# Optimization experiments

Hardware: AMD Instinct MI355X
Metric: run time of the kernel (lower is better)

Reference implementation:

```python
import jax, jax.numpy as jnp
import numpy as np

B, NPQ, NPV, NSL, K, ED, H = 64, 1024, 256, 1, 128, 16, 8
DK = K // H  # per-head dim (k_dim = v_dim = emb_dim // num_heads)
ETYPES = [("PQ","PQ"),("PQ","PV"),("PQ","Slack"),("PV","PQ"),("PV","PV"),("PV","Slack"),("Slack","PQ"),("Slack","PV")]
ECOUNTS = [262144, 131072, 4096, 131072, 65536, 2048, 4096, 2048]
NN = {"PQ": B*NPQ, "PV": B*NPV, "Slack": B*NSL}
LN_EPS = 1e-5


def setup_inputs() -> dict:
    ks = iter(jax.random.split(jax.random.key(0), 64))
    inp = {}
    for name, n in [("x_PQ", NN["PQ"]), ("x_PV", NN["PV"]), ("x_Slack", NN["Slack"])]:
        inp[name] = jax.random.normal(next(ks), (n, K), jnp.float32)
    for t, ((s, d), E) in enumerate(zip(ETYPES, ECOUNTS)):
        src = jax.random.randint(next(ks), (E,), 0, NN[s])
        dst = jax.random.randint(next(ks), (E,), 0, NN[d])
        inp[f"ei_{t}"] = jnp.stack([src, dst]).astype(jnp.int32)
        inp[f"ea_{t}"] = jax.random.normal(next(ks), (E, ED), jnp.float32)
    sc = 1.0 / np.sqrt(K)
    shapes = {"Wk": (2,8,K,K), "bk": (2,8,K), "Wq": (2,8,K,K), "bq": (2,8,K),
              "Wv": (2,8,K,K), "bv": (2,8,K), "Ws": (2,8,K,K), "bconv": (2,8,K),
              "We": (2,8,ED,K), "be": (2,8,K), "Wgt": (K,K), "bgt": (K,),
              "Wq1": (K,K), "Wk2": (K,K), "Wv2": (K,K), "Wo": (K,K), "bo": (K,)}
    for name, sh in shapes.items():
        inp[name] = jax.random.normal(next(ks), sh, jnp.float32) * sc
    inp["ln_g"] = jnp.ones((K,), jnp.float32)
    inp["ln_b"] = jnp.zeros((K,), jnp.float32)
    return inp


def _cross_attention(x1, x2, Wq1, Wk2, Wv2, Wo, bo):
    # x1: [B, N1, K] queries; x2: [B, N2, K] keys/values
    Bq, N1, _ = x1.shape
    N2 = x2.shape[1]
    q = (x1 @ Wq1).reshape(Bq, N1, H, DK)
    k = (x2 @ Wk2).reshape(Bq, N2, H, DK)
    v = (x2 @ Wv2).reshape(Bq, N2, H, DK)
    attn = jnp.einsum("bnhd,bmhd->bhnm", q, k) / np.sqrt(DK).astype(np.float32)
    attn = jax.nn.softmax(attn, axis=-1)
    out = jnp.einsum("bhnm,bmhd->bnhd", attn, v).reshape(Bq, N1, H * DK)
    return out @ Wo + bo


def _forward(x_PQ, x_PV, x_Slack, ei, ea,
             Wk, bk, Wq, bq, Wv, bv, Ws, bconv, We, be,
             Wgt, bgt, Wq1, Wk2, Wv2, Wo, bo, ln_g, ln_b):
    x = {"PQ": x_PQ, "PV": x_PV, "Slack": x_Slack}
    # global feature from input node features
    gf = jnp.concatenate([x_PQ.reshape(B, NPQ, K),
                          x_PV.reshape(B, NPV, K),
                          x_Slack.reshape(B, NSL, K)], axis=1)
    gf = gf @ Wgt + bgt
    gnode = jnp.concatenate([gf.mean(axis=1, keepdims=True),
                             gf.max(axis=1, keepdims=True)], axis=1)  # [B, 2, K]
    # 2 HeteroConv layers of ResGatedGraphConv, aggr='sum' over edge types
    for l in range(2):
        new = {t: jnp.zeros((NN[t], K), x_PQ.dtype) for t in ("PQ", "PV", "Slack")}
        for t, (s, d) in enumerate(ETYPES):
            xs, xd = x[s], x[d]
            k_ = xd @ Wk[l, t] + bk[l, t]   # lin_key on dst
            q_ = xs @ Wq[l, t] + bq[l, t]   # lin_query on src
            v_ = xs @ Wv[l, t] + bv[l, t]   # lin_value on src
            e_ = ea[t] @ We[l, t] + be[l, t]  # lin_edge
            si, di = ei[t][0], ei[t][1]
            gate = jax.nn.sigmoid(k_[di] + q_[si] + e_)  # [E, K]
            agg = jax.ops.segment_sum(gate * v_[si], di, num_segments=NN[d])
            new[d] = new[d] + agg + xd @ Ws[l, t] + bconv[l, t]
        x = {t: jax.nn.relu(v) for t, v in new.items()}
    # cross-attention vs. global mean/max nodes, residual, layernorm (PQ, PV only)
    res = {}
    for key2, N1 in (("PQ", NPQ), ("PV", NPV)):
        x1 = x[key2].reshape(B, N1, K)
        ca = _cross_attention(x1, gnode, Wq1, Wk2, Wv2, Wo, bo).reshape(B * N1, K)
        h = x[key2] + ca
        mu = h.mean(axis=-1, keepdims=True)
        var = ((h - mu) ** 2).mean(axis=-1, keepdims=True)
        res[key2] = (h - mu) * jax.lax.rsqrt(var + LN_EPS) * ln_g + ln_b
    return res["PQ"], res["PV"], x["Slack"]


def reference(x_PQ, x_PV, x_Slack,
              ei_0, ei_1, ei_2, ei_3, ei_4, ei_5, ei_6, ei_7,
              ea_0, ea_1, ea_2, ea_3, ea_4, ea_5, ea_6, ea_7,
              Wk, bk, Wq, bq, Wv, bv, Ws, bconv, We, be,
              Wgt, bgt, Wq1, Wk2, Wv2, Wo, bo, ln_g, ln_b):
    ei = [ei_0, ei_1, ei_2, ei_3, ei_4, ei_5, ei_6, ei_7]
    ea = [ea_0, ea_1, ea_2, ea_3, ea_4, ea_5, ea_6, ea_7]
    return _forward(x_PQ, x_PV, x_Slack, ei, ea,
                    Wk, bk, Wq, bq, Wv, bv, Ws, bconv, We, be,
                    Wgt, bgt, Wq1, Wk2, Wv2, Wo, bo, ln_g, ln_b)
```

## Files before the change

kernel.cpp:

```cpp
#include <hip/hip_runtime.h>
#include <hip/hip_bf16.h>
#include <math.h>

#define N_PQ 65536
#define N_PV 16384
#define N_SL 64

typedef __attribute__((ext_vector_type(8))) short s16x8;
typedef __attribute__((ext_vector_type(4))) float f32x4;

__device__ __forceinline__ ushort f2bf(float f) {
    union { float f; unsigned u; } x; x.f = f;
    unsigned r = x.u + 0x7fff + ((x.u >> 16) & 1);
    return (ushort)(r >> 16);
}
__device__ __forceinline__ float bf2f(ushort u) {
    union { unsigned u; float f; } x; x.u = ((unsigned)u) << 16;
    return x.f;
}

template<int OUT_BF16>
__global__ __launch_bounds__(256) void gemm_mfma(
    const ushort* __restrict__ A, const ushort* __restrict__ Bt,
    const float* __restrict__ bias, void* __restrict__ Cv, int M, int N)
{
    __shared__ ushort As[128 * 128];
    const int tid = threadIdx.x;
    const int m0 = blockIdx.x * 128;
    const int n0 = blockIdx.y * 128;

    #pragma unroll
    for (int p = 0; p < 8; ++p) {
        int c = p * 256 + tid;
        int row = c >> 4, c16 = c & 15;
        int gr = m0 + row;
        int4 v = make_int4(0, 0, 0, 0);
        if (gr < M) v = *(const int4*)(A + (size_t)gr * 128 + c16 * 8);
        *(int4*)(As + row * 128 + (c16 ^ (row & 7)) * 8) = v;
    }
    __syncthreads();

    const int lane = tid & 63, wave = tid >> 6;
    const int wr = wave >> 1, wc = wave & 1;
    const int lrow = lane & 15, lk = lane >> 4;

    f32x4 acc[4][4];
    #pragma unroll
    for (int mi = 0; mi < 4; ++mi)
        #pragma unroll
        for (int ni = 0; ni < 4; ++ni) acc[mi][ni] = (f32x4){0.f, 0.f, 0.f, 0.f};

    #pragma unroll
    for (int kk = 0; kk < 4; ++kk) {
        s16x8 a[4], b[4];
        #pragma unroll
        for (int mi = 0; mi < 4; ++mi) {
            int row = wr * 64 + mi * 16 + lrow;
            int c16 = (lk + kk * 4) ^ (row & 7);
            a[mi] = *(const s16x8*)(As + row * 128 + c16 * 8);
        }
        #pragma unroll
        for (int ni = 0; ni < 4; ++ni) {
            int n = n0 + wc * 64 + ni * 16 + lrow;
            b[ni] = *(const s16x8*)(Bt + (size_t)n * 128 + kk * 32 + lk * 8);
        }
        #pragma unroll
        for (int mi = 0; mi < 4; ++mi)
            #pragma unroll
            for (int ni = 0; ni < 4; ++ni)
                acc[mi][ni] = __builtin_amdgcn_mfma_f32_16x16x32_bf16(
                    a[mi], b[ni], acc[mi][ni], 0, 0, 0);
    }

    if (OUT_BF16) {
        __syncthreads();
        ushort* Cl = As;
        #pragma unroll
        for (int mi = 0; mi < 4; ++mi)
            #pragma unroll
            for (int ni = 0; ni < 4; ++ni)
                #pragma unroll
                for (int r = 0; r < 4; ++r) {
                    int row = wr * 64 + mi * 16 + (lane >> 4) * 4 + r;
                    int col = wc * 64 + ni * 16 + (lane & 15);
                    float v = acc[mi][ni][r] + (bias ? bias[n0 + col] : 0.f);
                    Cl[row * 128 + (((col >> 3) ^ (row & 7)) << 3) + (col & 7)] = f2bf(v);
                }
        __syncthreads();
        ushort* C = (ushort*)Cv;
        #pragma unroll
        for (int p = 0; p < 8; ++p) {
            int c = p * 256 + tid;
            int row = c >> 4, c16 = c & 15;
            int gr = m0 + row;
            if (gr < M)
                *(int4*)(C + (size_t)gr * N + n0 + c16 * 8) =
                    *(const int4*)(As + row * 128 + (c16 ^ (row & 7)) * 8);
        }
    } else {
        float* C = (float*)Cv;
        #pragma unroll
        for (int mi = 0; mi < 4; ++mi)
            #pragma unroll
            for (int ni = 0; ni < 4; ++ni)
                #pragma unroll
                for (int r = 0; r < 4; ++r) {
                    int row = m0 + wr * 64 + mi * 16 + (lane >> 4) * 4 + r;
                    int col = n0 + wc * 64 + ni * 16 + (lane & 15);
                    if (row < M)
                        C[(size_t)row * N + col] =
                            acc[mi][ni][r] + (bias ? bias[col] : 0.f);
                }
    }
}

__global__ void prep_mats(
    const float* __restrict__ Wk, const float* __restrict__ Wq,
    const float* __restrict__ Wv, const float* __restrict__ Ws,
    const float* __restrict__ Wgt, const float* __restrict__ Wq1,
    const float* __restrict__ Wk2, const float* __restrict__ Wv2,
    const float* __restrict__ Wo,
    ushort* __restrict__ panels, ushort* __restrict__ wssum,
    ushort* __restrict__ finalw)
{
    const int m = blockIdx.x >> 6;
    const int e = (blockIdx.x & 63) * 256 + threadIdx.x;
    const int nl = e >> 7, k = e & 127;
    const int dstlist[3][3] = {{0,3,6},{1,4,7},{2,5,-1}};
    const int srclist[3][3] = {{0,1,2},{3,4,5},{6,7,-1}};
    const int nkg[3] = {3,3,2};
    const int gofs[3] = {0,1280,2560};

    if (m < 52) {
        int l = m / 26, r = m % 26;
        int g, slot;
        if (r < 10)      { g = 0; slot = r; }
        else if (r < 20) { g = 1; slot = r - 10; }
        else             { g = 2; slot = r - 20; }
        int nk = nkg[g];
        float val; int col;
        if (slot < nk) {
            int t = dstlist[g][slot];
            val = Wk[(size_t)(l * 8 + t) * 16384 + k * 128 + nl];
            col = slot * 128 + nl;
        } else if (slot < 2 * nk) {
            int s = slot - nk; int t = srclist[g][s];
            val = Wq[(size_t)(l * 8 + t) * 16384 + k * 128 + nl];
            col = nk * 128 + s * 256 + ((nl >> 1) << 2) + (nl & 1);
        } else if (slot < 3 * nk) {
            int s = slot - 2 * nk; int t = srclist[g][s];
            val = Wv[(size_t)(l * 8 + t) * 16384 + k * 128 + nl];
            col = nk * 128 + s * 256 + ((nl >> 1) << 2) + 2 + (nl & 1);
        } else {
            float s = 0.f;
            #pragma unroll
            for (int i = 0; i < 3; ++i) {
                int t = dstlist[g][i];
                if (t >= 0) s += Ws[(size_t)(l * 8 + t) * 16384 + k * 128 + nl];
            }
            val = s; col = 1152 + nl;
        }
        panels[((size_t)l * 3328 + gofs[g] + col) * 128 + k] = f2bf(val);
    } else if (m < 54) {
        int l = m - 52;
        float s = Ws[(size_t)(l * 8 + 2) * 16384 + k * 128 + nl]
                + Ws[(size_t)(l * 8 + 5) * 16384 + k * 128 + nl];
        wssum[(size_t)l * 16384 + nl * 128 + k] = f2bf(s);
    } else {
        const float* fsrc[5] = {Wgt, Wq1, Wk2, Wv2, Wo};
        int idx = m - 54;
        finalw[(size_t)idx * 16384 + nl * 128 + k] = f2bf(fsrc[idx][k * 128 + nl]);
    }
}

__global__ void prep_bias(
    const float* __restrict__ bk, const float* __restrict__ bq,
    const float* __restrict__ bv, const float* __restrict__ bconv,
    float* __restrict__ bias_cat, float* __restrict__ bcsum)
{
    const int l = blockIdx.x / 3, g = blockIdx.x % 3;
    const int dstlist[3][3] = {{0,3,6},{1,4,7},{2,5,-1}};
    const int srclist[3][3] = {{0,1,2},{3,4,5},{6,7,-1}};
    const int nkg[3] = {3,3,2};
    const int gofs[3] = {0,1280,2560};
    const int nslots = (g < 2) ? 10 : 6;
    int nk = nkg[g];
    for (int idx = threadIdx.x; idx < nslots * 128; idx += 256) {
        int slot = idx >> 7, nl = idx & 127;
        float val; int col;
        if (slot < nk) {
            int t = dstlist[g][slot];
            val = bk[(l * 8 + t) * 128 + nl];
            col = slot * 128 + nl;
        } else if (slot < 2 * nk) {
            int s = slot - nk; int t = srclist[g][s];
            val = bq[(l * 8 + t) * 128 + nl];
            col = nk * 128 + s * 256 + ((nl >> 1) << 2) + (nl & 1);
        } else if (slot < 3 * nk) {
            int s = slot - 2 * nk; int t = srclist[g][s];
            val = bv[(l * 8 + t) * 128 + nl];
            col = nk * 128 + s * 256 + ((nl >> 1) << 2) + 2 + (nl & 1);
        } else {
            float s = 0.f;
            #pragma unroll
            for (int i = 0; i < 3; ++i) {
                int t = dstlist[g][i];
                if (t >= 0) s += bconv[(l * 8 + t) * 128 + nl];
            }
            val = s; col = 1152 + nl;
        }
        bias_cat[l * 3328 + gofs[g] + col] = val;
    }
    if (g == 2 && threadIdx.x < 128) {
        bcsum[l * 128 + threadIdx.x] =
            bconv[(l * 8 + 2) * 128 + threadIdx.x] + bconv[(l * 8 + 5) * 128 + threadIdx.x];
    }
}

struct HArgs {
    const int* ei[6];
    int E[6];
    int base[6];
    int cum[7];
};

__global__ void hist_kernel(HArgs A, int* __restrict__ bins)
{
    int g = blockIdx.x * 256 + threadIdx.x;
    if (g >= A.cum[6]) return;
    int t = 0;
    #pragma unroll
    for (int i = 0; i < 5; ++i) t += (g >= A.cum[i + 1]);
    int e = g - A.cum[t];
    int dst = A.ei[t][A.E[t] + e];
    atomicAdd(&bins[A.base[t] + dst], 1);
}

__global__ __launch_bounds__(256) void scan_a(
    const int* __restrict__ bins, int* __restrict__ offs, int* __restrict__ bsum)
{
    __shared__ int s[256];
    const int b = blockIdx.x, t = threadIdx.x;
    int v = bins[b * 256 + t];
    s[t] = v; __syncthreads();
    #pragma unroll
    for (int off = 1; off < 256; off <<= 1) {
        int x = (t >= off) ? s[t - off] : 0;
        __syncthreads();
        s[t] += x;
        __syncthreads();
    }
    offs[b * 256 + t] = s[t] - v;
    if (t == 255) bsum[b] = s[255];
}

__global__ __launch_bounds__(1024) void scan_b(
    const int* __restrict__ bsum, int* __restrict__ carry)
{
    __shared__ int s[1024];
    const int t = threadIdx.x;
    int v = bsum[t];
    s[t] = v; __syncthreads();
    for (int off = 1; off < 1024; off <<= 1) {
        int x = (t >= off) ? s[t - off] : 0;
        __syncthreads();
        s[t] += x;
        __syncthreads();
    }
    carry[t] = s[t] - v;
}

__global__ void scan_c(int* __restrict__ offs, const int* __restrict__ carry,
                       int* __restrict__ cursor)
{
    const int b = blockIdx.x, t = threadIdx.x;
    int v = offs[b * 256 + t] + carry[b];
    offs[b * 256 + t] = v;
    cursor[b * 256 + t] = v;
}

__global__ void scatter_kernel(HArgs A, int* __restrict__ cursor,
                               int* __restrict__ lsrc, int* __restrict__ leid)
{
    int g = blockIdx.x * 256 + threadIdx.x;
    if (g >= A.cum[6]) return;
    int t = 0;
    #pragma unroll
    for (int i = 0; i < 5; ++i) t += (g >= A.cum[i + 1]);
    int e = g - A.cum[t];
    int src = A.ei[t][e];
    int dst = A.ei[t][A.E[t] + e];
    int pos = atomicAdd(&cursor[A.base[t] + dst], 1);
    lsrc[pos] = src;
    leid[pos] = e;
}

struct GTA {
    int base, kcol, qvcol, lds;
    const ushort* Ys;
    const float* ea;
    const float* We;
    const float* be;
};
struct GArgs {
    GTA t[3];
    const int* offs;
    const int* lsrc;
    const int* leid;
    ushort* xbg;
    const ushort* Yg;
    int ldg, wscol;
};

__global__ __launch_bounds__(256) void gather_kernel(GArgs A)
{
    const int wave = threadIdx.x >> 6, lane = threadIdx.x & 63;
    const int d = blockIdx.x * 4 + wave;
    const int j0 = lane * 2;

    ushort2 w2 = *(const ushort2*)(A.Yg + (size_t)d * A.ldg + A.wscol + j0);
    float a0 = bf2f(w2.x), a1 = bf2f(w2.y);

    #pragma unroll
    for (int i = 0; i < 3; ++i) {
        const GTA T = A.t[i];
        int start = __builtin_amdgcn_readfirstlane(A.offs[T.base + d]);
        int end   = __builtin_amdgcn_readfirstlane(A.offs[T.base + d + 1]);
        if (start == end) continue;

        ushort2 kk = *(const ushort2*)(A.Yg + (size_t)d * A.ldg + T.kcol + j0);
        float k0 = bf2f(kk.x), k1 = bf2f(kk.y);
        float we0[16], we1[16];
        #pragma unroll
        for (int r = 0; r < 16; ++r) {
            float2 wv = *(const float2*)(T.We + r * 128 + j0);
            we0[r] = wv.x; we1[r] = wv.y;
        }
        float2 be2 = *(const float2*)(T.be + j0);

        int si  = __builtin_amdgcn_readfirstlane(A.lsrc[start]);
        int eid = __builtin_amdgcn_readfirstlane(A.leid[start]);
        uint2 qv = *(const uint2*)(T.Ys + (size_t)si * T.lds + T.qvcol + lane * 4);
        float4 eA = *(const float4*)(T.ea + (size_t)eid * 16);
        float4 eB = *(const float4*)(T.ea + (size_t)eid * 16 + 4);
        float4 eC = *(const float4*)(T.ea + (size_t)eid * 16 + 8);
        float4 eD = *(const float4*)(T.ea + (size_t)eid * 16 + 12);

        for (int e = start; e < end; ++e) {
            int nx = (e + 1 < end) ? (e + 1) : e;
            int si_n  = __builtin_amdgcn_readfirstlane(A.lsrc[nx]);
            int eid_n = __builtin_amdgcn_readfirstlane(A.leid[nx]);
            uint2 qv_n = *(const uint2*)(T.Ys + (size_t)si_n * T.lds + T.qvcol + lane * 4);
            float4 nA = *(const float4*)(T.ea + (size_t)eid_n * 16);
            float4 nB = *(const float4*)(T.ea + (size_t)eid_n * 16 + 4);
            float4 nC = *(const float4*)(T.ea + (size_t)eid_n * 16 + 8);
            float4 nD = *(const float4*)(T.ea + (size_t)eid_n * 16 + 12);

            float e0 = be2.x, e1 = be2.y;
            e0 += eA.x*we0[0] + eA.y*we0[1] + eA.z*we0[2] + eA.w*we0[3]
                + eB.x*we0[4] + eB.y*we0[5] + eB.z*we0[6] + eB.w*we0[7]
                + eC.x*we0[8] + eC.y*we0[9] + eC.z*we0[10] + eC.w*we0[11]
                + eD.x*we0[12] + eD.y*we0[13] + eD.z*we0[14] + eD.w*we0[15];
            e1 += eA.x*we1[0] + eA.y*we1[1] + eA.z*we1[2] + eA.w*we1[3]
                + eB.x*we1[4] + eB.y*we1[5] + eB.z*we1[6] + eB.w*we1[7]
                + eC.x*we1[8] + eC.y*we1[9] + eC.z*we1[10] + eC.w*we1[11]
                + eD.x*we1[12] + eD.y*we1[13] + eD.z*we1[14] + eD.w*we1[15];
            float q0 = bf2f((ushort)(qv.x & 0xffff)), q1 = bf2f((ushort)(qv.x >> 16));
            float v0 = bf2f((ushort)(qv.y & 0xffff)), v1 = bf2f((ushort)(qv.y >> 16));
            float g0 = 1.f / (1.f + __expf(-(k0 + q0 + e0)));
            float g1 = 1.f / (1.f + __expf(-(k1 + q1 + e1)));
            a0 += g0 * v0;
            a1 += g1 * v1;
            qv = qv_n; eA = nA; eB = nB; eC = nC; eD = nD;
        }
    }
    ushort2 o; o.x = f2bf(fmaxf(a0, 0.f)); o.y = f2bf(fmaxf(a1, 0.f));
    *(ushort2*)(A.xbg + (size_t)d * 128 + j0) = o;
}

__global__ __launch_bounds__(256) void edge_slack(
    const int* __restrict__ ei, const float* __restrict__ ea,
    const float* __restrict__ We, const float* __restrict__ be,
    const ushort* __restrict__ Yk, int ldk,
    const ushort* __restrict__ Yqv, int ldq,
    float* __restrict__ nd, int E)
{
    const int e = blockIdx.x * 2 + (threadIdx.x >> 7);
    if (e >= E) return;
    const int j = threadIdx.x & 127;
    const int si = ei[e];
    const int di = ei[E + e];

    float ej = be[j];
    #pragma unroll
    for (int r = 0; r < 16; ++r)
        ej += ea[(size_t)e * 16 + r] * We[r * 128 + j];

    float kv = bf2f(Yk[(size_t)di * ldk + j]);
    float qv = bf2f(Yqv[(size_t)si * ldq + ((j >> 1) << 2) + (j & 1)]);
    float vv = bf2f(Yqv[(size_t)si * ldq + ((j >> 1) << 2) + 2 + (j & 1)]);
    float g  = 1.f / (1.f + __expf(-(kv + qv + ej)));
    atomicAdd(&nd[(size_t)di * 128 + j], g * vv);
}

__global__ void f2b_kernel(const float* __restrict__ a, ushort* __restrict__ o, int n)
{
    int i = (blockIdx.x * 256 + threadIdx.x) * 4;
    if (i < n) {
        float4 v = *(const float4*)(a + i);
        ushort4 u; u.x = f2bf(v.x); u.y = f2bf(v.y); u.z = f2bf(v.z); u.w = f2bf(v.w);
        *(ushort4*)(o + i) = u;
    }
}
__global__ void relu_b_kernel(const float* __restrict__ a, ushort* __restrict__ o, int n)
{
    int i = (blockIdx.x * 256 + threadIdx.x) * 4;
    if (i < n) {
        float4 v = *(const float4*)(a + i);
        ushort4 u;
        u.x = f2bf(fmaxf(v.x, 0.f)); u.y = f2bf(fmaxf(v.y, 0.f));
        u.z = f2bf(fmaxf(v.z, 0.f)); u.w = f2bf(fmaxf(v.w, 0.f));
        *(ushort4*)(o + i) = u;
    }
}
__global__ void b2f_kernel(const ushort* __restrict__ a, float* __restrict__ o, int n)
{
    int i = blockIdx.x * 256 + threadIdx.x;
    if (i < n) o[i] = bf2f(a[i]);
}

__global__ void pool1(const ushort* __restrict__ gf, float* __restrict__ pbuf)
{
    const int b = blockIdx.x >> 4, c = blockIdx.x & 15;
    const int j = threadIdx.x;
    float s = 0.f, m = -INFINITY;
    const ushort* pq = gf + (size_t)(b * 1024 + c * 64) * 128;
    for (int i = 0; i < 64; ++i) { float v = bf2f(pq[i * 128 + j]); s += v; m = fmaxf(m, v); }
    const ushort* pv = gf + (size_t)(N_PQ + b * 256 + c * 16) * 128;
    for (int i = 0; i < 16; ++i) { float v = bf2f(pv[i * 128 + j]); s += v; m = fmaxf(m, v); }
    if (c == 0) { float v = bf2f(gf[(size_t)(N_PQ + N_PV + b) * 128 + j]); s += v; m = fmaxf(m, v); }
    pbuf[(size_t)blockIdx.x * 256 + j] = s;
    pbuf[(size_t)blockIdx.x * 256 + 128 + j] = m;
}
__global__ void pool2(const float* __restrict__ pbuf, float* __restrict__ gnode)
{
    const int b = blockIdx.x, j = threadIdx.x;
    float s = 0.f, m = -INFINITY;
    for (int c = 0; c < 16; ++c) {
        s += pbuf[(size_t)(b * 16 + c) * 256 + j];
        m = fmaxf(m, pbuf[(size_t)(b * 16 + c) * 256 + 128 + j]);
    }
    gnode[(size_t)(b * 2) * 128 + j]     = s * (1.f / 1281.f);
    gnode[(size_t)(b * 2 + 1) * 128 + j] = m;
}

__global__ __launch_bounds__(256) void attn_kernel(
    const ushort* __restrict__ q, const float* __restrict__ k2,
    const float* __restrict__ v2, ushort* __restrict__ ao, int shift, int Ntot)
{
    const int n = blockIdx.x * 2 + (threadIdx.x >> 7);
    if (n >= Ntot) return;
    const int j = threadIdx.x & 127;
    const int b = n >> shift;
    const int h16 = j & ~15;

    const ushort* qn = q + (size_t)n * 128 + h16;
    const float* k0 = k2 + (size_t)(b * 2) * 128 + h16;
    const float* k1 = k2 + (size_t)(b * 2 + 1) * 128 + h16;
    float s0 = 0.f, s1 = 0.f;
    #pragma unroll
    for (int d = 0; d < 16; ++d) {
        float qq = bf2f(qn[d]); s0 += qq * k0[d]; s1 += qq * k1[d];
    }
    s0 *= 0.25f; s1 *= 0.25f;
    float m  = fmaxf(s0, s1);
    float a0 = __expf(s0 - m), a1 = __expf(s1 - m);
    float inv = 1.f / (a0 + a1);
    ao[(size_t)n * 128 + j] = f2bf(
        (a0 * v2[(size_t)(b * 2) * 128 + j] + a1 * v2[(size_t)(b * 2 + 1) * 128 + j]) * inv);
}

__global__ __launch_bounds__(256) void ln_kernel(
    const ushort* __restrict__ x, const float* __restrict__ ca,
    const float* __restrict__ g, const float* __restrict__ bb,
    float* __restrict__ out, int N)
{
    const int n = blockIdx.x * 4 + (threadIdx.x >> 6);
    if (n >= N) return;
    const int l = threadIdx.x & 63;
    const size_t base = (size_t)n * 128;
    float h0 = bf2f(x[base + l * 2])     + ca[base + l * 2];
    float h1 = bf2f(x[base + l * 2 + 1]) + ca[base + l * 2 + 1];
    float s  = h0 + h1;
    float ss = h0 * h0 + h1 * h1;
    #pragma unroll
    for (int o = 32; o; o >>= 1) { s += __shfl_xor(s, o); ss += __shfl_xor(ss, o); }
    float mu  = s * (1.f / 128.f);
    float var = ss * (1.f / 128.f) - mu * mu;
    float rs  = rsqrtf(var + 1e-5f);
    out[base + l * 2]     = (h0 - mu) * rs * g[l * 2]     + bb[l * 2];
    out[base + l * 2 + 1] = (h1 - mu) * rs * g[l * 2 + 1] + bb[l * 2 + 1];
}

extern "C" void kernel_launch(void* const* d_in, const int* in_sizes, int n_in,
                              void* d_out, int out_size, void* d_ws, size_t ws_size,
                              hipStream_t stream)
{
    const float* xin[3] = {(const float*)d_in[0], (const float*)d_in[1], (const float*)d_in[2]};
    const int NNs[3] = {N_PQ, N_PV, N_SL};
    const int ncol[3] = {1280, 1280, 768};
    const int gofs[3] = {0, 1280, 2560};

    const int*   ei[8];
    const float* ea[8];
    int          Ecnt[8];
    for (int t = 0; t < 8; ++t) {
        ei[t]   = (const int*)d_in[3 + 2 * t];
        ea[t]   = (const float*)d_in[4 + 2 * t];
        Ecnt[t] = in_sizes[3 + 2 * t] / 2;
    }
    const float* Wk    = (const float*)d_in[19];
    const float* bk    = (const float*)d_in[20];
    const float* Wq    = (const float*)d_in[21];
    const float* bq    = (const float*)d_in[22];
    const float* Wv    = (const float*)d_in[23];
    const float* bv    = (const float*)d_in[24];
    const float* Ws    = (const float*)d_in[25];
    const float* bconv = (const float*)d_in[26];
    const float* We    = (const float*)d_in[27];
    const float* be    = (const float*)d_in[28];
    const float* Wgt   = (const float*)d_in[29];
    const float* bgt   = (const float*)d_in[30];
    const float* Wq1   = (const float*)d_in[31];
    const float* Wk2   = (const float*)d_in[32];
    const float* Wv2   = (const float*)d_in[33];
    const float* Wo    = (const float*)d_in[34];
    const float* bo    = (const float*)d_in[35];
    const float* ln_g  = (const float*)d_in[36];
    const float* ln_b  = (const float*)d_in[37];

    char* w = (char*)d_ws;
    ushort* Y[3];
    Y[0] = (ushort*)w; w += (size_t)N_PQ * 1280 * 2;
    Y[1] = (ushort*)w; w += (size_t)N_PV * 1280 * 2;
    Y[2] = (ushort*)w; w += (size_t)N_SL * 768 * 2;
    ushort* xb[3];
    xb[0] = (ushort*)w; w += (size_t)N_PQ * 128 * 2;
    xb[1] = (ushort*)w; w += (size_t)N_PV * 128 * 2;
    xb[2] = (ushort*)w; w += (size_t)N_SL * 128 * 2;
    ushort* panels = (ushort*)w; w += (size_t)2 * 3328 * 128 * 2;
    ushort* wssum  = (ushort*)w; w += (size_t)2 * 16384 * 2;
    ushort* finalw = (ushort*)w; w += (size_t)5 * 16384 * 2;
    float* bias_cat = (float*)w; w += 6656 * 4;
    float* bcsum    = (float*)w; w += 256 * 4;
    float* gnode    = (float*)w; w += 16384 * 4;
    ushort* gnodeb  = (ushort*)w; w += 16384 * 2;
    float* k2       = (float*)w; w += 16384 * 4;
    float* v2       = (float*)w; w += 16384 * 4;
    float* pbuf     = (float*)w; w += 1024 * 256 * 4;
    const int NBINS = 262144;
    int* bins   = (int*)w; w += (size_t)NBINS * 4;
    int* offs   = (int*)w; w += (size_t)NBINS * 4;
    int* cursor = (int*)w; w += (size_t)NBINS * 4;
    int* bsum   = (int*)w; w += 1024 * 4;
    int* carry  = (int*)w; w += 1024 * 4;
    int* lsrc   = (int*)w; w += (size_t)600064 * 4;
    int* leid   = (int*)w; w += (size_t)600064 * 4;
    ushort* gf   = Y[0];
    ushort* qb   = Y[0];
    ushort* ao   = (ushort*)((char*)Y[0] + (size_t)N_PQ * 128 * 2);
    float*  cbuf = (float*)((char*)Y[0] + (size_t)N_PQ * 128 * 4);
    float* outp = (float*)d_out;
    float* nw2 = outp + (size_t)(N_PQ + N_PV) * 128;

    const ushort* Wgt_t = finalw;
    const ushort* Wq1_t = finalw + 16384;
    const ushort* Wk2_t = finalw + 32768;
    const ushort* Wv2_t = finalw + 49152;
    const ushort* Wo_t  = finalw + 65536;

    auto gemm_b = [&](const ushort* A, const ushort* Bt, const float* bias,
                      ushort* C, int M, int N) {
        gemm_mfma<1><<<dim3((M + 127) / 128, N / 128), 256, 0, stream>>>(A, Bt, bias, C, M, N);
    };
    auto gemm_f = [&](const ushort* A, const ushort* Bt, const float* bias,
                      float* C, int M, int N) {
        gemm_mfma<0><<<dim3((M + 127) / 128, N / 128), 256, 0, stream>>>(A, Bt, bias, C, M, N);
    };

    prep_mats<<<59 * 64, 256, 0, stream>>>(Wk, Wq, Wv, Ws, Wgt, Wq1, Wk2, Wv2, Wo,
                                           panels, wssum, finalw);
    prep_bias<<<6, 256, 0, stream>>>(bk, bq, bv, bconv, bias_cat, bcsum);
    for (int g = 0; g < 3; ++g) {
        int n = NNs[g] * 128;
        f2b_kernel<<<dim3((n / 4 + 255) / 256), 256, 0, stream>>>(xin[g], xb[g], n);
    }

    const int csr_t[6]    = {0, 3, 6, 1, 4, 7};
    const int csr_base[6] = {0, 65536, 131072, 196608, 212992, 229376};
    HArgs ha;
    {
        int c = 0;
        for (int i = 0; i < 6; ++i) {
            int t = csr_t[i];
            ha.ei[i] = ei[t]; ha.E[i] = Ecnt[t]; ha.base[i] = csr_base[i];
            ha.cum[i] = c; c += Ecnt[t];
        }
        ha.cum[6] = c;
    }
    hipMemsetAsync(bins, 0, (size_t)NBINS * 4, stream);
    hist_kernel<<<dim3((ha.cum[6] + 255) / 256), 256, 0, stream>>>(ha, bins);
    scan_a<<<1024, 256, 0, stream>>>(bins, offs, bsum);
    scan_b<<<1, 1024, 0, stream>>>(bsum, carry);
    scan_c<<<1024, 256, 0, stream>>>(offs, carry, cursor);
    scatter_kernel<<<dim3((ha.cum[6] + 255) / 256), 256, 0, stream>>>(ha, cursor, lsrc, leid);

    gemm_b(xb[0], Wgt_t, bgt, gf, N_PQ, 128);
    gemm_b(xb[1], Wgt_t, bgt, gf + (size_t)N_PQ * 128, N_PV, 128);
    gemm_b(xb[2], Wgt_t, bgt, gf + (size_t)(N_PQ + N_PV) * 128, N_SL, 128);
    pool1<<<1024, 128, 0, stream>>>(gf, pbuf);
    pool2<<<64, 128, 0, stream>>>(pbuf, gnode);
    f2b_kernel<<<dim3(16384 / 4 / 256), 256, 0, stream>>>(gnode, gnodeb, 16384);
    gemm_f(gnodeb, Wk2_t, nullptr, k2, 128, 128);
    gemm_f(gnodeb, Wv2_t, nullptr, v2, 128, 128);

    for (int l = 0; l < 2; ++l) {
        for (int g = 0; g < 3; ++g)
            gemm_b(xb[g], panels + ((size_t)l * 3328 + gofs[g]) * 128,
                   bias_cat + l * 3328 + gofs[g], Y[g], NNs[g], ncol[g]);
        gemm_f(xb[2], wssum + (size_t)l * 16384, bcsum + l * 128, nw2, N_SL, 128);

        for (int g = 0; g < 2; ++g) {
            GArgs ga;
            for (int i = 0; i < 3; ++i) {
                int t = csr_t[g * 3 + i], off = l * 8 + t;
                int sgrp = (i == 2) ? 2 : i;
                ga.t[i].base  = csr_base[g * 3 + i];
                ga.t[i].kcol  = i * 128;
                ga.t[i].lds   = ncol[sgrp];
                ga.t[i].qvcol = ((sgrp == 2) ? 256 : 384) + g * 256;
                ga.t[i].Ys    = Y[sgrp];
                ga.t[i].ea    = ea[t];
                ga.t[i].We    = We + (size_t)off * 2048;
                ga.t[i].be    = be + (size_t)off * 128;
            }
            ga.offs = offs; ga.lsrc = lsrc; ga.leid = leid;
            ga.xbg = xb[g]; ga.Yg = Y[g]; ga.ldg = ncol[g]; ga.wscol = 1152;
            gather_kernel<<<dim3(NNs[g] / 4), 256, 0, stream>>>(ga);
        }

        {
            int off2 = l * 8 + 2;
            edge_slack<<<dim3((Ecnt[2] + 1) / 2), 256, 0, stream>>>(
                ei[2], ea[2], We + (size_t)off2 * 2048, be + (size_t)off2 * 128,
                Y[2] + 0, 768, Y[0] + 896, 1280, nw2, Ecnt[2]);
            int off5 = l * 8 + 5;
            edge_slack<<<dim3((Ecnt[5] + 1) / 2), 256, 0, stream>>>(
                ei[5], ea[5], We + (size_t)off5 * 2048, be + (size_t)off5 * 128,
                Y[2] + 128, 768, Y[1] + 896, 1280, nw2, Ecnt[5]);
        }
        relu_b_kernel<<<dim3(8), 256, 0, stream>>>(nw2, xb[2], N_SL * 128);
    }

    gemm_b(xb[0], Wq1_t, nullptr, qb, N_PQ, 128);
    attn_kernel<<<dim3(N_PQ / 2), 256, 0, stream>>>(qb, k2, v2, ao, 10, N_PQ);
    gemm_f(ao, Wo_t, bo, cbuf, N_PQ, 128);
    ln_kernel<<<dim3(N_PQ / 4), 256, 0, stream>>>(xb[0], cbuf, ln_g, ln_b, outp, N_PQ);
    gemm_b(xb[1], Wq1_t, nullptr, qb, N_PV, 128);
    attn_kernel<<<dim3(N_PV / 2), 256, 0, stream>>>(qb, k2, v2, ao, 8, N_PV);
    gemm_f(ao, Wo_t, bo, cbuf, N_PV, 128);
    ln_kernel<<<dim3(N_PV / 4), 256, 0, stream>>>(xb[1], cbuf, ln_g, ln_b,
                                                  outp + (size_t)N_PQ * 128, N_PV);
    b2f_kernel<<<dim3((N_SL * 128 + 255) / 256), 256, 0, stream>>>(
        xb[2], outp + (size_t)(N_PQ + N_PV) * 128, N_SL * 128);
}
```

Measured before the change: 985.1 us.

## Double-buffer edge prefetch in gather and batch GEMMs across node types

The gather loop now keeps two edges in flight with separate prefetch buffers, so more independent loads overlap with the sigmoid/FMA work per node. Separately, the Wgt, Wq1, Wo GEMMs and the layernorm are merged into single launches covering PQ, PV (and Slack) rows. This relies on xb[0..2] being contiguous in memory, and the ao/cbuf scratch offsets are moved to make room. Fewer launches and tail waves are traded for more registers in the gather kernel and a layout assumption.

```diff
diff --git a/kernel.cpp b/kernel.cpp
--- a/kernel.cpp
+++ b/kernel.cpp
@@ -338,41 +338,67 @@
         }
         float2 be2 = *(const float2*)(T.be + j0);
 
-        int si  = __builtin_amdgcn_readfirstlane(A.lsrc[start]);
-        int eid = __builtin_amdgcn_readfirstlane(A.leid[start]);
-        uint2 qv = *(const uint2*)(T.Ys + (size_t)si * T.lds + T.qvcol + lane * 4);
-        float4 eA = *(const float4*)(T.ea + (size_t)eid * 16);
-        float4 eB = *(const float4*)(T.ea + (size_t)eid * 16 + 4);
-        float4 eC = *(const float4*)(T.ea + (size_t)eid * 16 + 8);
-        float4 eD = *(const float4*)(T.ea + (size_t)eid * 16 + 12);
-
-        for (int e = start; e < end; ++e) {
-            int nx = (e + 1 < end) ? (e + 1) : e;
-            int si_n  = __builtin_amdgcn_readfirstlane(A.lsrc[nx]);
-            int eid_n = __builtin_amdgcn_readfirstlane(A.leid[nx]);
-            uint2 qv_n = *(const uint2*)(T.Ys + (size_t)si_n * T.lds + T.qvcol + lane * 4);
-            float4 nA = *(const float4*)(T.ea + (size_t)eid_n * 16);
-            float4 nB = *(const float4*)(T.ea + (size_t)eid_n * 16 + 4);
-            float4 nC = *(const float4*)(T.ea + (size_t)eid_n * 16 + 8);
-            float4 nD = *(const float4*)(T.ea + (size_t)eid_n * 16 + 12);
-
-            float e0 = be2.x, e1 = be2.y;
-            e0 += eA.x*we0[0] + eA.y*we0[1] + eA.z*we0[2] + eA.w*we0[3]
-                + eB.x*we0[4] + eB.y*we0[5] + eB.z*we0[6] + eB.w*we0[7]
-                + eC.x*we0[8] + eC.y*we0[9] + eC.z*we0[10] + eC.w*we0[11]
-                + eD.x*we0[12] + eD.y*we0[13] + eD.z*we0[14] + eD.w*we0[15];
-            e1 += eA.x*we1[0] + eA.y*we1[1] + eA.z*we1[2] + eA.w*we1[3]
-                + eB.x*we1[4] + eB.y*we1[5] + eB.z*we1[6] + eB.w*we1[7]
-                + eC.x*we1[8] + eC.y*we1[9] + eC.z*we1[10] + eC.w*we1[11]
-                + eD.x*we1[12] + eD.y*we1[13] + eD.z*we1[14] + eD.w*we1[15];
-            float q0 = bf2f((ushort)(qv.x & 0xffff)), q1 = bf2f((ushort)(qv.x >> 16));
-            float v0 = bf2f((ushort)(qv.y & 0xffff)), v1 = bf2f((ushort)(qv.y >> 16));
-            float g0 = 1.f / (1.f + __expf(-(k0 + q0 + e0)));
-            float g1 = 1.f / (1.f + __expf(-(k1 + q1 + e1)));
-            a0 += g0 * v0;
-            a1 += g1 * v1;
-            qv = qv_n; eA = nA; eB = nB; eC = nC; eD = nD;
-        }
+        int eB = (start + 1 < end) ? start + 1 : start;
+        int siA  = __builtin_amdgcn_readfirstlane(A.lsrc[start]);
+        int eidA = __builtin_amdgcn_readfirstlane(A.leid[start]);
+        uint2 qvA = *(const uint2*)(T.Ys + (size_t)siA * T.lds + T.qvcol + lane * 4);
+        float4 aA0 = *(const float4*)(T.ea + (size_t)eidA * 16);
+        float4 aA1 = *(const float4*)(T.ea + (size_t)eidA * 16 + 4);
+        float4 aA2 = *(const float4*)(T.ea + (size_t)eidA * 16 + 8);
+        float4 aA3 = *(const float4*)(T.ea + (size_t)eidA * 16 + 12);
+        int siB  = __builtin_amdgcn_readfirstlane(A.lsrc[eB]);
+        int eidB = __builtin_amdgcn_readfirstlane(A.leid[eB]);
+        uint2 qvB = *(const uint2*)(T.Ys + (size_t)siB * T.lds + T.qvcol + lane * 4);
+        float4 aB0 = *(const float4*)(T.ea + (size_t)eidB * 16);
+        float4 aB1 = *(const float4*)(T.ea + (size_t)eidB * 16 + 4);
+        float4 aB2 = *(const float4*)(T.ea + (size_t)eidB * 16 + 8);
+        float4 aB3 = *(const float4*)(T.ea + (size_t)eidB * 16 + 12);
+
+        #define COMPUTE(QV, C0, C1, C2, C3) { \
+            float e0 = be2.x, e1 = be2.y; \
+            e0 += (C0).x*we0[0] + (C0).y*we0[1] + (C0).z*we0[2] + (C0).w*we0[3] \
+                + (C1).x*we0[4] + (C1).y*we0[5] + (C1).z*we0[6] + (C1).w*we0[7] \
+                + (C2).x*we0[8] + (C2).y*we0[9] + (C2).z*we0[10] + (C2).w*we0[11] \
+                + (C3).x*we0[12] + (C3).y*we0[13] + (C3).z*we0[14] + (C3).w*we0[15]; \
+            e1 += (C0).x*we1[0] + (C0).y*we1[1] + (C0).z*we1[2] + (C0).w*we1[3] \
+                + (C1).x*we1[4] + (C1).y*we1[5] + (C1).z*we1[6] + (C1).w*we1[7] \
+                + (C2).x*we1[8] + (C2).y*we1[9] + (C2).z*we1[10] + (C2).w*we1[11] \
+                + (C3).x*we1[12] + (C3).y*we1[13] + (C3).z*we1[14] + (C3).w*we1[15]; \
+            float q0 = bf2f((ushort)((QV).x & 0xffff)), q1 = bf2f((ushort)((QV).x >> 16)); \
+            float v0 = bf2f((ushort)((QV).y & 0xffff)), v1 = bf2f((ushort)((QV).y >> 16)); \
+            float g0 = 1.f / (1.f + __expf(-(k0 + q0 + e0))); \
+            float g1 = 1.f / (1.f + __expf(-(k1 + q1 + e1))); \
+            a0 = fmaf(g0, v0, a0); \
+            a1 = fmaf(g1, v1, a1); }
+
+        for (int e = start; e < end; e += 2) {
+            uint2 qc = qvA;
+            float4 c0 = aA0, c1 = aA1, c2 = aA2, c3 = aA3;
+            int nxA = (e + 2 < end) ? e + 2 : e;
+            siA  = __builtin_amdgcn_readfirstlane(A.lsrc[nxA]);
+            eidA = __builtin_amdgcn_readfirstlane(A.leid[nxA]);
+            qvA = *(const uint2*)(T.Ys + (size_t)siA * T.lds + T.qvcol + lane * 4);
+            aA0 = *(const float4*)(T.ea + (size_t)eidA * 16);
+            aA1 = *(const float4*)(T.ea + (size_t)eidA * 16 + 4);
+            aA2 = *(const float4*)(T.ea + (size_t)eidA * 16 + 8);
+            aA3 = *(const float4*)(T.ea + (size_t)eidA * 16 + 12);
+            COMPUTE(qc, c0, c1, c2, c3)
+
+            if (e + 1 < end) {
+                uint2 qc2 = qvB;
+                float4 d0 = aB0, d1 = aB1, d2 = aB2, d3 = aB3;
+                int nxB = (e + 3 < end) ? e + 3 : e;
+                siB  = __builtin_amdgcn_readfirstlane(A.lsrc[nxB]);
+                eidB = __builtin_amdgcn_readfirstlane(A.leid[nxB]);
+                qvB = *(const uint2*)(T.Ys + (size_t)siB * T.lds + T.qvcol + lane * 4);
+                aB0 = *(const float4*)(T.ea + (size_t)eidB * 16);
+                aB1 = *(const float4*)(T.ea + (size_t)eidB * 16 + 4);
+                aB2 = *(const float4*)(T.ea + (size_t)eidB * 16 + 8);
+                aB3 = *(const float4*)(T.ea + (size_t)eidB * 16 + 12);
+                COMPUTE(qc2, d0, d1, d2, d3)
+            }
+        }
+        #undef COMPUTE
     }
     ushort2 o; o.x = f2bf(fmaxf(a0, 0.f)); o.y = f2bf(fmaxf(a1, 0.f));
     *(ushort2*)(A.xbg + (size_t)d * 128 + j0) = o;
@@ -568,8 +594,8 @@
     int* leid   = (int*)w; w += (size_t)600064 * 4;
     ushort* gf   = Y[0];
     ushort* qb   = Y[0];
-    ushort* ao   = (ushort*)((char*)Y[0] + (size_t)N_PQ * 128 * 2);
-    float*  cbuf = (float*)((char*)Y[0] + (size_t)N_PQ * 128 * 4);
+    ushort* ao   = Y[0] + (size_t)81920 * 128;
+    float*  cbuf = (float*)(Y[0] + (size_t)2 * 81920 * 128);
     float* outp = (float*)d_out;
     float* nw2 = outp + (size_t)(N_PQ + N_PV) * 128;
 
@@ -615,9 +641,7 @@
     scan_c<<<1024, 256, 0, stream>>>(offs, carry, cursor);
     scatter_kernel<<<dim3((ha.cum[6] + 255) / 256), 256, 0, stream>>>(ha, cursor, lsrc, leid);
 
-    gemm_b(xb[0], Wgt_t, bgt, gf, N_PQ, 128);
-    gemm_b(xb[1], Wgt_t, bgt, gf + (size_t)N_PQ * 128, N_PV, 128);
-    gemm_b(xb[2], Wgt_t, bgt, gf + (size_t)(N_PQ + N_PV) * 128, N_SL, 128);
+    gemm_b(xb[0], Wgt_t, bgt, gf, N_PQ + N_PV + N_SL, 128);
     pool1<<<1024, 128, 0, stream>>>(gf, pbuf);
     pool2<<<64, 128, 0, stream>>>(pbuf, gnode);
     f2b_kernel<<<dim3(16384 / 4 / 256), 256, 0, stream>>>(gnode, gnodeb, 16384);
@@ -662,15 +686,13 @@
         relu_b_kernel<<<dim3(8), 256, 0, stream>>>(nw2, xb[2], N_SL * 128);
     }
 
-    gemm_b(xb[0], Wq1_t, nullptr, qb, N_PQ, 128);
+    gemm_b(xb[0], Wq1_t, nullptr, qb, N_PQ + N_PV, 128);
     attn_kernel<<<dim3(N_PQ / 2), 256, 0, stream>>>(qb, k2, v2, ao, 10, N_PQ);
-    gemm_f(ao, Wo_t, bo, cbuf, N_PQ, 128);
-    ln_kernel<<<dim3(N_PQ / 4), 256, 0, stream>>>(xb[0], cbuf, ln_g, ln_b, outp, N_PQ);
-    gemm_b(xb[1], Wq1_t, nullptr, qb, N_PV, 128);
-    attn_kernel<<<dim3(N_PV / 2), 256, 0, stream>>>(qb, k2, v2, ao, 8, N_PV);
-    gemm_f(ao, Wo_t, bo, cbuf, N_PV, 128);
-    ln_kernel<<<dim3(N_PV / 4), 256, 0, stream>>>(xb[1], cbuf, ln_g, ln_b,
-                                                  outp + (size_t)N_PQ * 128, N_PV);
+    attn_kernel<<<dim3(N_PV / 2), 256, 0, stream>>>(qb + (size_t)N_PQ * 128, k2, v2,
+                                                    ao + (size_t)N_PQ * 128, 8, N_PV);
+    gemm_f(ao, Wo_t, bo, cbuf, N_PQ + N_PV, 128);
+    ln_kernel<<<dim3((N_PQ + N_PV) / 4), 256, 0, stream>>>(xb[0], cbuf, ln_g, ln_b,
+                                                           outp, N_PQ + N_PV);
     b2f_kernel<<<dim3((N_SL * 128 + 255) / 256), 256, 0, stream>>>(
         xb[2], outp + (size_t)(N_PQ + N_PV) * 128, N_SL * 128);
 }
```

Measured after the change: 910.8 us. -7.5%, faster.
